# Kernel tuning notes

Measured on AMD Instinct MI355X. Metric: run time of the kernel, lower is better.

The kernel has to match this reference:

```python
import jax, jax.numpy as jnp
import numpy as np

N = 100000   # nodes
E = 1600000  # edges (avg degree 16)
F_IN, F_HID, F_OUT = 64, 64, 16


def setup_inputs() -> dict:
    key = jax.random.key(0)
    ks = jax.random.split(key, 10)
    features = jax.random.normal(ks[0], (N, F_IN), dtype=jnp.float32)
    src = jax.random.randint(ks[1], (E,), 0, N, dtype=jnp.int32)
    dst = jax.random.randint(ks[2], (E,), 0, N, dtype=jnp.int32)
    # Xavier-uniform weights, zero bias (matches nn.init in the module)
    def xavier(k, fan_in, fan_out):
        lim = np.sqrt(6.0 / (fan_in + fan_out))
        return jax.random.uniform(k, (fan_in, fan_out), jnp.float32, -lim, lim)
    return {
        "features": features,
        "W1": xavier(ks[3], F_IN, F_HID), "b1": jnp.zeros((F_HID,), jnp.float32),
        "W2": xavier(ks[4], F_HID, F_HID), "b2": jnp.zeros((F_HID,), jnp.float32),
        "W3": xavier(ks[5], F_HID, F_OUT), "b3": jnp.zeros((F_OUT,), jnp.float32),
        "src": src, "dst": dst,
    }


def pairnorm_scs(x):
    # PairNorm 'PN-SCS', scale=1
    col_mean = x.mean(axis=0)                                    # [F]
    rownorm = jnp.sqrt(1e-6 + jnp.sum(x * x, axis=1, keepdims=True))  # [N,1]
    return x / rownorm - col_mean


def graph_conv(h, src, dst, W, b):
    # copy_u('h','m') + sum reduce over edges, plus self-loop
    agg = jax.ops.segment_sum(h[src], dst, num_segments=N) + h   # [N,F]
    return agg @ W + b


def reference(features, W1, b1, W2, b2, W3, b3, src, dst):
    h = features
    for W, b in ((W1, b1), (W2, b2)):
        h = pairnorm_scs(h)
        h = jax.nn.relu(graph_conv(h, src, dst, W, b))
        # dropout p=0.0 -> identity
    return graph_conv(h, src, dst, W3, b3)
```

## Files before the change

### kernel.cpp

```cpp
#include <hip/hip_runtime.h>


#define NHB 64

__device__ __forceinline__ unsigned short f2bf(float f) {
  unsigned u = __builtin_bit_cast(unsigned, f);
  u += 0x7FFFu + ((u >> 16) & 1u);
  return (unsigned short)(u >> 16);
}
__device__ __forceinline__ float bf2f(unsigned short h) {
  return __builtin_bit_cast(float, ((unsigned)h) << 16);
}

__global__ void colsum_kernel(const float* __restrict__ x, float* __restrict__ cs,
                              int n4, int relu) {
  __shared__ float lds[16][64];
  float s0 = 0.f, s1 = 0.f, s2 = 0.f, s3 = 0.f;
  const int t = threadIdx.x;
  const int stride = gridDim.x * blockDim.x;
  for (int i = blockIdx.x * blockDim.x + t; i < n4; i += stride) {
    float4 v = ((const float4*)x)[i];
    if (relu) {
      v.x = fmaxf(v.x, 0.f); v.y = fmaxf(v.y, 0.f);
      v.z = fmaxf(v.z, 0.f); v.w = fmaxf(v.w, 0.f);
    }
    s0 += v.x; s1 += v.y; s2 += v.z; s3 += v.w;
  }
  const int r = t >> 4;
  const int cq = (t & 15) * 4;
  lds[r][cq + 0] = s0; lds[r][cq + 1] = s1; lds[r][cq + 2] = s2; lds[r][cq + 3] = s3;
  __syncthreads();
  if (t < 64) {
    float tot = 0.f;
    #pragma unroll
    for (int rr = 0; rr < 16; ++rr) tot += lds[rr][t];
    unsafeAtomicAdd(&cs[t], tot);
  }
}

__global__ __launch_bounds__(256) void matnorm_kernel(
    const float* x, const float* __restrict__ W,
    const float* __restrict__ cs, unsigned short* __restrict__ z,
    int N, int relu_in, float invN) {
  const int lane = threadIdx.x & 63;
  const int wid  = blockIdx.x * (blockDim.x >> 6) + (threadIdx.x >> 6);
  const int nw   = gridDim.x * (blockDim.x >> 6);

  float w[64];
  float cm = 0.f;
  #pragma unroll
  for (int k = 0; k < 64; ++k) {
    w[k] = W[k * 64 + lane];
    cm = fmaf(cs[k], w[k], cm);
  }
  cm *= invN;

  for (int row = wid; row < N; row += nw) {
    float xv = x[(size_t)row * 64 + lane];
    if (relu_in) xv = fmaxf(xv, 0.f);
    float ss = xv * xv;
    #pragma unroll
    for (int m = 1; m < 64; m <<= 1) ss += __shfl_xor(ss, m, 64);
    const float rinv = 1.0f / sqrtf(1e-6f + ss);
    float acc = 0.f;
    #pragma unroll
    for (int k = 0; k < 64; ++k) {
      const float xk = __builtin_bit_cast(
          float, __builtin_amdgcn_readlane(__builtin_bit_cast(int, xv), k));
      acc = fmaf(xk, w[k], acc);
    }
    z[(size_t)row * 64 + lane] = f2bf(acc * rinv - cm);
  }
}

__global__ __launch_bounds__(256) void mat16_kernel(
    const float* __restrict__ x, const float* __restrict__ W3,
    unsigned short* __restrict__ z3, int N) {
  const int lane = threadIdx.x & 63;
  const int j = lane & 15;
  const int wid = blockIdx.x * (blockDim.x >> 6) + (threadIdx.x >> 6);
  const int nw  = gridDim.x * (blockDim.x >> 6);

  float w[64];
  #pragma unroll
  for (int k = 0; k < 64; ++k) w[k] = W3[k * 16 + j];
  for (int row = wid; row < N; row += nw) {
    const float xv = fmaxf(x[(size_t)row * 64 + lane], 0.f);
    float acc = 0.f;
    #pragma unroll
    for (int k = 0; k < 64; ++k) {
      const float xk = __builtin_bit_cast(
          float, __builtin_amdgcn_readlane(__builtin_bit_cast(int, xv), k));
      acc = fmaf(xk, w[k], acc);
    }
    if (lane < 16) z3[(size_t)row * 16 + lane] = f2bf(acc);
  }
}


__global__ __launch_bounds__(256) void countA_kernel(
    const int* __restrict__ dst, int* __restrict__ cntA, int E) {
  __shared__ int lc[NHB];
  if (threadIdx.x < NHB) lc[threadIdx.x] = 0;
  __syncthreads();
  const int stride = gridDim.x * blockDim.x;
  for (int e = blockIdx.x * blockDim.x + threadIdx.x; e < E; e += stride)
    atomicAdd(&lc[__builtin_nontemporal_load(&dst[e]) >> 11], 1);
  __syncthreads();
  if (threadIdx.x < NHB && lc[threadIdx.x])
    atomicAdd(&cntA[threadIdx.x], lc[threadIdx.x]);
}

__global__ void scanA_kernel(const int* __restrict__ cntA,
                             int* __restrict__ baseA, int* __restrict__ curA,
                             int NHI) {
  if (threadIdx.x == 0) {
    int acc = 0;
    for (int p = 0; p < NHI; ++p) { baseA[p] = acc; curA[p] = acc; acc += cntA[p]; }
    baseA[NHI] = acc;
  }
}

#define TILE 2048
#define CAPA 96
__global__ __launch_bounds__(256) void scatterA_kernel(
    const int* __restrict__ src, const int* __restrict__ dst,
    int* __restrict__ curA, int* __restrict__ psrc, int* __restrict__ pdst,
    int E) {
  __shared__ int lss[NHB][CAPA], ldd[NHB][CAPA];
  __shared__ int lcnt[NHB], lbase[NHB];
  const int t = threadIdx.x;
  if (t < NHB) lcnt[t] = 0;
  __syncthreads();
  const int ntiles = (E + TILE - 1) / TILE;
  for (int tile = blockIdx.x; tile < ntiles; tile += gridDim.x) {
    const int base = tile * TILE;
    #pragma unroll
    for (int j = 0; j < TILE / 256; ++j) {
      const int e = base + j * 256 + t;
      if (e < E) {
        const int d = __builtin_nontemporal_load(&dst[e]);
        const int s = __builtin_nontemporal_load(&src[e]);
        const int p = d >> 11;
        const int slot = atomicAdd(&lcnt[p], 1);
        if (slot < CAPA) { lss[p][slot] = s; ldd[p][slot] = d; }
        else {
          const int pos = atomicAdd(&curA[p], 1);
          psrc[pos] = s; pdst[pos] = d;
        }
      }
    }
    __syncthreads();
    if (t < NHB) {
      int c = lcnt[t]; if (c > CAPA) c = CAPA;
      lbase[t] = c ? atomicAdd(&curA[t], c) : 0;
      lcnt[t] = c;
    }
    __syncthreads();
    for (int p = 0; p < NHB; ++p) {
      const int c = lcnt[p];
      if (t < c) {
        psrc[lbase[p] + t] = lss[p][t];
        pdst[lbase[p] + t] = ldd[p][t];
      }
    }
    __syncthreads();
    if (t < NHB) lcnt[t] = 0;
    __syncthreads();
  }
}

__global__ __launch_bounds__(1024) void fillsort_kernel(
    const int* __restrict__ psrc, const int* __restrict__ pdst,
    const int* __restrict__ baseA, int* __restrict__ rowstart,
    int* __restrict__ csr, int N, int E) {
  __shared__ int hist[2048];
  __shared__ int bs[1024];
  const int t = threadIdx.x;
  const int h = blockIdx.x;
  const int nlo = h << 11;
  const int elo = baseA[h], ehi = baseA[h + 1];

  for (int i = t; i < 2048; i += 1024) hist[i] = 0;
  __syncthreads();

  int e = elo + t;
  for (; e + 3 * 1024 < ehi; e += 4 * 1024) {
    const int d0 = pdst[e], d1 = pdst[e + 1024],
              d2 = pdst[e + 2048], d3 = pdst[e + 3072];
    atomicAdd(&hist[d0 - nlo], 1); atomicAdd(&hist[d1 - nlo], 1);
    atomicAdd(&hist[d2 - nlo], 1); atomicAdd(&hist[d3 - nlo], 1);
  }
  for (; e < ehi; e += 1024) atomicAdd(&hist[pdst[e] - nlo], 1);
  __syncthreads();

  const int c0 = hist[2 * t], c1 = hist[2 * t + 1];
  const int s = c0 + c1;
  bs[t] = s;
  __syncthreads();
  for (int off = 1; off < 1024; off <<= 1) {
    const int v = (t >= off) ? bs[t - off] : 0;
    __syncthreads();
    bs[t] += v;
    __syncthreads();
  }
  const int excl = bs[t] - s;

  const int n0 = nlo + 2 * t;
  hist[2 * t] = excl;
  hist[2 * t + 1] = excl + c0;
  if (n0 < N)     rowstart[n0]     = elo + excl;
  if (n0 + 1 < N) rowstart[n0 + 1] = elo + excl + c0;
  if (h == 0 && t == 0) rowstart[N] = E;
  __syncthreads();

  e = elo + t;
  for (; e + 3 * 1024 < ehi; e += 4 * 1024) {
    const int d0 = pdst[e],        s0 = psrc[e];
    const int d1 = pdst[e + 1024], s1 = psrc[e + 1024];
    const int d2 = pdst[e + 2048], s2 = psrc[e + 2048];
    const int d3 = pdst[e + 3072], s3 = psrc[e + 3072];
    csr[elo + atomicAdd(&hist[d0 - nlo], 1)] = s0;
    csr[elo + atomicAdd(&hist[d1 - nlo], 1)] = s1;
    csr[elo + atomicAdd(&hist[d2 - nlo], 1)] = s2;
    csr[elo + atomicAdd(&hist[d3 - nlo], 1)] = s3;
  }
  for (; e < ehi; e += 1024) {
    const int d = pdst[e], sv = psrc[e];
    csr[elo + atomicAdd(&hist[d - nlo], 1)] = sv;
  }
}

__global__ __launch_bounds__(256) void gather64_kernel(
    const unsigned short* __restrict__ z, const float* __restrict__ b,
    const int* __restrict__ rowstart, const int* __restrict__ csr,
    float* __restrict__ agg, int N) {
  const int lane = threadIdx.x & 63;
  int node = blockIdx.x * (blockDim.x >> 6) + (threadIdx.x >> 6);
  if (node >= N) return;
  node = __builtin_amdgcn_readfirstlane(node);
  const int start = rowstart[node];
  const int end   = rowstart[node + 1];
  const unsigned short hs = z[(size_t)node * 64 + lane];
  float a0 = 0.f, a1 = 0.f, a2 = 0.f, a3 = 0.f;
  int e = start;
  for (; e + 16 <= end; e += 16) {
    unsigned short h[16];
    #pragma unroll
    for (int j = 0; j < 16; ++j) h[j] = z[(size_t)csr[e + j] * 64 + lane];
    #pragma unroll
    for (int j = 0; j < 16; j += 4) {
      a0 += bf2f(h[j + 0]); a1 += bf2f(h[j + 1]);
      a2 += bf2f(h[j + 2]); a3 += bf2f(h[j + 3]);
    }
  }
  for (; e + 4 <= end; e += 4) {
    unsigned short h[4];
    #pragma unroll
    for (int j = 0; j < 4; ++j) h[j] = z[(size_t)csr[e + j] * 64 + lane];
    a0 += bf2f(h[0]); a1 += bf2f(h[1]); a2 += bf2f(h[2]); a3 += bf2f(h[3]);
  }
  for (; e < end; ++e) a0 += bf2f(z[(size_t)csr[e] * 64 + lane]);
  const float sum = (a0 + a1) + (a2 + a3);
  agg[(size_t)node * 64 + lane] = bf2f(hs) + b[lane] + sum;
}

__global__ __launch_bounds__(256) void gather16_kernel(
    const unsigned short* __restrict__ z3, const float* __restrict__ b3,
    const int* __restrict__ rowstart, const int* __restrict__ csr,
    float* __restrict__ out, int N) {
  const int lane = threadIdx.x & 63;
  const int f = lane & 15;
  const int g = lane >> 4;
  int node = blockIdx.x * (blockDim.x >> 6) + (threadIdx.x >> 6);
  if (node >= N) return;
  node = __builtin_amdgcn_readfirstlane(node);
  const int start = rowstart[node];
  const int end   = rowstart[node + 1];
  float acc0 = 0.f, acc1 = 0.f;
  int e = start + g;
  for (; e + 4 < end; e += 8) {
    acc0 += bf2f(z3[(size_t)csr[e] * 16 + f]);
    acc1 += bf2f(z3[(size_t)csr[e + 4] * 16 + f]);
  }
  if (e < end) acc0 += bf2f(z3[(size_t)csr[e] * 16 + f]);
  float acc = acc0 + acc1;
  acc += __shfl_xor(acc, 16, 64);
  acc += __shfl_xor(acc, 32, 64);
  if (lane < 16)
    out[(size_t)node * 16 + f] = bf2f(z3[(size_t)node * 16 + f]) + b3[f] + acc;
}

extern "C" void kernel_launch(void* const* d_in, const int* in_sizes, int n_in,
                              void* d_out, int out_size, void* d_ws, size_t ws_size,
                              hipStream_t stream) {
  const float* feat = (const float*)d_in[0];
  const float* W1 = (const float*)d_in[1];
  const float* b1 = (const float*)d_in[2];
  const float* W2 = (const float*)d_in[3];
  const float* b2 = (const float*)d_in[4];
  const float* W3 = (const float*)d_in[5];
  const float* b3 = (const float*)d_in[6];
  const int* src = (const int*)d_in[7];
  const int* dst = (const int*)d_in[8];
  const int N = in_sizes[0] / 64;
  const int E = in_sizes[7];
  float* out = (float*)d_out;

  float* B            = (float*)d_ws;
  unsigned short* zb  = (unsigned short*)(B + (size_t)N * 64);
  unsigned short* z3b = zb + (size_t)N * 64;
  int* cntA  = (int*)(z3b + (size_t)N * 16);
  float* cs1 = (float*)(cntA + NHB);
  float* cs2 = cs1 + 64;
  int* baseA    = (int*)(cs2 + 64);
  int* curA     = baseA + NHB + 1;
  int* rowstart = curA + NHB;
  int* csr      = rowstart + N + 1;
  int* psrc = (int*)zb;
  int* pdst = psrc + E;

  const int NHI = (N + 2047) >> 11;
  const int node_blocks = (N + 3) / 4;
  const float invN = 1.0f / (float)N;

  hipMemsetAsync(cntA, 0, (NHB + 128) * sizeof(int), stream);
  countA_kernel<<<512, 256, 0, stream>>>(dst, cntA, E);
  scanA_kernel<<<1, 64, 0, stream>>>(cntA, baseA, curA, NHI);
  scatterA_kernel<<<512, 256, 0, stream>>>(src, dst, curA, psrc, pdst, E);
  fillsort_kernel<<<NHI, 1024, 0, stream>>>(psrc, pdst, baseA, rowstart, csr, N, E);

  colsum_kernel<<<512, 256, 0, stream>>>(feat, cs1, N * 16, 0);
  matnorm_kernel<<<1024, 256, 0, stream>>>(feat, W1, cs1, zb, N, 0, invN);
  gather64_kernel<<<node_blocks, 256, 0, stream>>>(zb, b1, rowstart, csr, B, N);

  colsum_kernel<<<512, 256, 0, stream>>>(B, cs2, N * 16, 1);
  matnorm_kernel<<<1024, 256, 0, stream>>>(B, W2, cs2, zb, N, 1, invN);
  gather64_kernel<<<node_blocks, 256, 0, stream>>>(zb, b2, rowstart, csr, B, N);

  mat16_kernel<<<1024, 256, 0, stream>>>(B, W3, z3b, N);
  gather16_kernel<<<node_blocks, 256, 0, stream>>>(z3b, b3, rowstart, csr, out, N);
}
```

Before: 436.6 us.

## Fuse column sums and ReLU into gather and prelude, process node pairs

Merges the edge-count histogram with the first-layer column sum in one prelude kernel. The ReLU and the second column sum now happen in the gather64 epilogue, so the separate colsum pass and the relu flags in matnorm and mat16 go away. gather64 becomes a grid-stride kernel where each wave handles two nodes at once, interleaving their neighbour loads for more memory-level parallelism. The cost is a shared-memory reduction plus atomics per block in the gather, and possible imbalance when the two paired nodes have different degrees.

```diff
diff --git a/kernel.cpp b/kernel.cpp
--- a/kernel.cpp
+++ b/kernel.cpp
@@ -12,24 +12,28 @@
   return __builtin_bit_cast(float, ((unsigned)h) << 16);
 }
 
-__global__ void colsum_kernel(const float* __restrict__ x, float* __restrict__ cs,
-                              int n4, int relu) {
+__global__ __launch_bounds__(256) void prelude_kernel(
+    const int* __restrict__ dst, int* __restrict__ cntA, int E,
+    const float* __restrict__ x, float* __restrict__ cs, int n4) {
+  __shared__ int lc[NHB];
   __shared__ float lds[16][64];
+  const int t = threadIdx.x;
+  if (t < NHB) lc[t] = 0;
+  __syncthreads();
+  const int stride = gridDim.x * blockDim.x;
+  for (int e = blockIdx.x * blockDim.x + t; e < E; e += stride)
+    atomicAdd(&lc[__builtin_nontemporal_load(&dst[e]) >> 11], 1);
+
   float s0 = 0.f, s1 = 0.f, s2 = 0.f, s3 = 0.f;
-  const int t = threadIdx.x;
-  const int stride = gridDim.x * blockDim.x;
   for (int i = blockIdx.x * blockDim.x + t; i < n4; i += stride) {
     float4 v = ((const float4*)x)[i];
-    if (relu) {
-      v.x = fmaxf(v.x, 0.f); v.y = fmaxf(v.y, 0.f);
-      v.z = fmaxf(v.z, 0.f); v.w = fmaxf(v.w, 0.f);
-    }
     s0 += v.x; s1 += v.y; s2 += v.z; s3 += v.w;
   }
   const int r = t >> 4;
   const int cq = (t & 15) * 4;
   lds[r][cq + 0] = s0; lds[r][cq + 1] = s1; lds[r][cq + 2] = s2; lds[r][cq + 3] = s3;
   __syncthreads();
+  if (t < NHB && lc[t]) atomicAdd(&cntA[t], lc[t]);
   if (t < 64) {
     float tot = 0.f;
     #pragma unroll
@@ -41,7 +45,7 @@
 __global__ __launch_bounds__(256) void matnorm_kernel(
     const float* x, const float* __restrict__ W,
     const float* __restrict__ cs, unsigned short* __restrict__ z,
-    int N, int relu_in, float invN) {
+    int N, float invN) {
   const int lane = threadIdx.x & 63;
   const int wid  = blockIdx.x * (blockDim.x >> 6) + (threadIdx.x >> 6);
   const int nw   = gridDim.x * (blockDim.x >> 6);
@@ -56,8 +60,7 @@
   cm *= invN;
 
   for (int row = wid; row < N; row += nw) {
-    float xv = x[(size_t)row * 64 + lane];
-    if (relu_in) xv = fmaxf(xv, 0.f);
+    const float xv = x[(size_t)row * 64 + lane];
     float ss = xv * xv;
     #pragma unroll
     for (int m = 1; m < 64; m <<= 1) ss += __shfl_xor(ss, m, 64);
@@ -85,7 +88,7 @@
   #pragma unroll
   for (int k = 0; k < 64; ++k) w[k] = W3[k * 16 + j];
   for (int row = wid; row < N; row += nw) {
-    const float xv = fmaxf(x[(size_t)row * 64 + lane], 0.f);
+    const float xv = x[(size_t)row * 64 + lane];
     float acc = 0.f;
     #pragma unroll
     for (int k = 0; k < 64; ++k) {
@@ -97,19 +100,6 @@
   }
 }
 
-
-__global__ __launch_bounds__(256) void countA_kernel(
-    const int* __restrict__ dst, int* __restrict__ cntA, int E) {
-  __shared__ int lc[NHB];
-  if (threadIdx.x < NHB) lc[threadIdx.x] = 0;
-  __syncthreads();
-  const int stride = gridDim.x * blockDim.x;
-  for (int e = blockIdx.x * blockDim.x + threadIdx.x; e < E; e += stride)
-    atomicAdd(&lc[__builtin_nontemporal_load(&dst[e]) >> 11], 1);
-  __syncthreads();
-  if (threadIdx.x < NHB && lc[threadIdx.x])
-    atomicAdd(&cntA[threadIdx.x], lc[threadIdx.x]);
-}
 
 __global__ void scanA_kernel(const int* __restrict__ cntA,
                              int* __restrict__ baseA, int* __restrict__ curA,
@@ -234,35 +224,84 @@
 __global__ __launch_bounds__(256) void gather64_kernel(
     const unsigned short* __restrict__ z, const float* __restrict__ b,
     const int* __restrict__ rowstart, const int* __restrict__ csr,
-    float* __restrict__ agg, int N) {
+    float* __restrict__ agg, float* __restrict__ csg, int N) {
   const int lane = threadIdx.x & 63;
-  int node = blockIdx.x * (blockDim.x >> 6) + (threadIdx.x >> 6);
-  if (node >= N) return;
-  node = __builtin_amdgcn_readfirstlane(node);
-  const int start = rowstart[node];
-  const int end   = rowstart[node + 1];
-  const unsigned short hs = z[(size_t)node * 64 + lane];
-  float a0 = 0.f, a1 = 0.f, a2 = 0.f, a3 = 0.f;
-  int e = start;
-  for (; e + 16 <= end; e += 16) {
-    unsigned short h[16];
-    #pragma unroll
-    for (int j = 0; j < 16; ++j) h[j] = z[(size_t)csr[e + j] * 64 + lane];
-    #pragma unroll
-    for (int j = 0; j < 16; j += 4) {
-      a0 += bf2f(h[j + 0]); a1 += bf2f(h[j + 1]);
-      a2 += bf2f(h[j + 2]); a3 += bf2f(h[j + 3]);
-    }
-  }
-  for (; e + 4 <= end; e += 4) {
-    unsigned short h[4];
-    #pragma unroll
-    for (int j = 0; j < 4; ++j) h[j] = z[(size_t)csr[e + j] * 64 + lane];
-    a0 += bf2f(h[0]); a1 += bf2f(h[1]); a2 += bf2f(h[2]); a3 += bf2f(h[3]);
-  }
-  for (; e < end; ++e) a0 += bf2f(z[(size_t)csr[e] * 64 + lane]);
-  const float sum = (a0 + a1) + (a2 + a3);
-  agg[(size_t)node * 64 + lane] = bf2f(hs) + b[lane] + sum;
+  const int wid  = blockIdx.x * (blockDim.x >> 6) + (threadIdx.x >> 6);
+  const int nw   = gridDim.x * (blockDim.x >> 6);
+  const float bl = b[lane];
+  float csum = 0.f;
+  const int npair = (N + 1) >> 1;
+
+  for (int p = wid; p < npair; p += nw) {
+    const int n0 = __builtin_amdgcn_readfirstlane(2 * p);
+    const int hasB = (n0 + 1 < N);
+    const int sA   = rowstart[n0];
+    const int eAend = rowstart[n0 + 1];
+    const int eBend = hasB ? rowstart[n0 + 2] : eAend;
+    const unsigned short hsA = z[(size_t)n0 * 64 + lane];
+    const unsigned short hsB = z[(size_t)(n0 + hasB) * 64 + lane];
+    float a0 = 0.f, a1 = 0.f, a2 = 0.f, a3 = 0.f;
+    float c0 = 0.f, c1 = 0.f, c2 = 0.f, c3 = 0.f;
+    int eA = sA, eB = eAend;
+    while (eA + 8 <= eAend && eB + 8 <= eBend) {
+      unsigned short hA[8], hB[8];
+      #pragma unroll
+      for (int j = 0; j < 8; ++j) hA[j] = z[(size_t)csr[eA + j] * 64 + lane];
+      #pragma unroll
+      for (int j = 0; j < 8; ++j) hB[j] = z[(size_t)csr[eB + j] * 64 + lane];
+      #pragma unroll
+      for (int j = 0; j < 8; j += 4) {
+        a0 += bf2f(hA[j]); a1 += bf2f(hA[j + 1]);
+        a2 += bf2f(hA[j + 2]); a3 += bf2f(hA[j + 3]);
+        c0 += bf2f(hB[j]); c1 += bf2f(hB[j + 1]);
+        c2 += bf2f(hB[j + 2]); c3 += bf2f(hB[j + 3]);
+      }
+      eA += 8; eB += 8;
+    }
+    for (; eA + 8 <= eAend; eA += 8) {
+      unsigned short hA[8];
+      #pragma unroll
+      for (int j = 0; j < 8; ++j) hA[j] = z[(size_t)csr[eA + j] * 64 + lane];
+      #pragma unroll
+      for (int j = 0; j < 8; j += 4) {
+        a0 += bf2f(hA[j]); a1 += bf2f(hA[j + 1]);
+        a2 += bf2f(hA[j + 2]); a3 += bf2f(hA[j + 3]);
+      }
+    }
+    for (; eA < eAend; ++eA) a0 += bf2f(z[(size_t)csr[eA] * 64 + lane]);
+    for (; eB + 8 <= eBend; eB += 8) {
+      unsigned short hB[8];
+      #pragma unroll
+      for (int j = 0; j < 8; ++j) hB[j] = z[(size_t)csr[eB + j] * 64 + lane];
+      #pragma unroll
+      for (int j = 0; j < 8; j += 4) {
+        c0 += bf2f(hB[j]); c1 += bf2f(hB[j + 1]);
+        c2 += bf2f(hB[j + 2]); c3 += bf2f(hB[j + 3]);
+      }
+    }
+    for (; eB < eBend; ++eB) c0 += bf2f(z[(size_t)csr[eB] * 64 + lane]);
+
+    const float oA = fmaxf(bf2f(hsA) + bl + ((a0 + a1) + (a2 + a3)), 0.f);
+    agg[(size_t)n0 * 64 + lane] = oA;
+    csum += oA;
+    if (hasB) {
+      const float oB = fmaxf(bf2f(hsB) + bl + ((c0 + c1) + (c2 + c3)), 0.f);
+      agg[(size_t)(n0 + 1) * 64 + lane] = oB;
+      csum += oB;
+    }
+  }
+
+  if (csg) {
+    __shared__ float lcs[4][64];
+    const int w = threadIdx.x >> 6;
+    lcs[w][lane] = csum;
+    __syncthreads();
+    if (threadIdx.x < 64) {
+      unsafeAtomicAdd(&csg[threadIdx.x],
+                      lcs[0][threadIdx.x] + lcs[1][threadIdx.x] +
+                      lcs[2][threadIdx.x] + lcs[3][threadIdx.x]);
+    }
+  }
 }
 
 __global__ __launch_bounds__(256) void gather16_kernel(
@@ -325,18 +364,16 @@
   const float invN = 1.0f / (float)N;
 
   hipMemsetAsync(cntA, 0, (NHB + 128) * sizeof(int), stream);
-  countA_kernel<<<512, 256, 0, stream>>>(dst, cntA, E);
+  prelude_kernel<<<512, 256, 0, stream>>>(dst, cntA, E, feat, cs1, N * 16);
   scanA_kernel<<<1, 64, 0, stream>>>(cntA, baseA, curA, NHI);
   scatterA_kernel<<<512, 256, 0, stream>>>(src, dst, curA, psrc, pdst, E);
   fillsort_kernel<<<NHI, 1024, 0, stream>>>(psrc, pdst, baseA, rowstart, csr, N, E);
 
-  colsum_kernel<<<512, 256, 0, stream>>>(feat, cs1, N * 16, 0);
-  matnorm_kernel<<<1024, 256, 0, stream>>>(feat, W1, cs1, zb, N, 0, invN);
-  gather64_kernel<<<node_blocks, 256, 0, stream>>>(zb, b1, rowstart, csr, B, N);
-
-  colsum_kernel<<<512, 256, 0, stream>>>(B, cs2, N * 16, 1);
-  matnorm_kernel<<<1024, 256, 0, stream>>>(B, W2, cs2, zb, N, 1, invN);
-  gather64_kernel<<<node_blocks, 256, 0, stream>>>(zb, b2, rowstart, csr, B, N);
+  matnorm_kernel<<<1024, 256, 0, stream>>>(feat, W1, cs1, zb, N, invN);
+  gather64_kernel<<<2048, 256, 0, stream>>>(zb, b1, rowstart, csr, B, cs2, N);
+
+  matnorm_kernel<<<1024, 256, 0, stream>>>(B, W2, cs2, zb, N, invN);
+  gather64_kernel<<<2048, 256, 0, stream>>>(zb, b2, rowstart, csr, B, nullptr, N);
 
   mat16_kernel<<<1024, 256, 0, stream>>>(B, W3, z3b, N);
   gather16_kernel<<<node_blocks, 256, 0, stream>>>(z3b, b3, rowstart, csr, out, N);
```

Measured after the change: 441.3 us. No clear change (+1.1%).
